# Kernel tuning notes

Measured on AMD Instinct MI355X. Metric: run time of the kernel, lower is better.

## Reference

```python
import jax, jax.numpy as jnp
import numpy as np

N, E, DIN, HID, H, ED = 50000, 800000, 128, 64, 4, 5
Z_IDX = 3          # impedance column
PHYS_W = 1.0       # physics_weight
NEG_SLOPE = 0.2    # GATv2 leaky_relu slope


def gat_layer(x, src, dst, ea, Wl, bl, Wr, br, We, att, temp, bias, concat):
    """PhysicsGATv2Conv (add_self_loops=False, eval mode / no dropout)."""
    n = x.shape[0]
    Hh, C = att.shape
    xl = (x @ Wl + bl).reshape(n, Hh, C)   # lin_l -> source features
    xr = (x @ Wr + br).reshape(n, Hh, C)   # lin_r -> target features
    # physics-enhanced edge attr: overwrite last column with temp * w / |Z|
    z = jnp.clip(ea[:, Z_IDX], 1e-6, None)
    ea = ea.at[:, -1].set(temp * PHYS_W / z)
    e = (ea @ We).reshape(-1, Hh, C)       # lin_edge (no bias)
    m = jax.nn.leaky_relu(xl[src] + xr[dst] + e, NEG_SLOPE)  # [E,H,C]
    logit = jnp.einsum('ehc,hc->eh', m, att)                 # [E,H]
    # segment softmax over incoming edges of each target node
    lmax = jax.ops.segment_max(logit, dst, num_segments=n)
    w = jnp.exp(logit - lmax[dst])
    den = jax.ops.segment_sum(w, dst, num_segments=n)
    a = w / (den[dst] + 1e-16)
    out = jax.ops.segment_sum(xl[src] * a[:, :, None], dst, num_segments=n)
    out = out.reshape(n, Hh * C) if concat else out.mean(axis=1)
    return out + bias


def layer_norm(x, w, b):
    mu = x.mean(-1, keepdims=True)
    v = ((x - mu) ** 2).mean(-1, keepdims=True)
    return (x - mu) * jax.lax.rsqrt(v + 1e-5) * w + b


def setup_inputs() -> dict:
    key = jax.random.key(0)
    ks = iter(jax.random.split(key, 40))
    nk = lambda: next(ks)
    d = {}
    d['x'] = jax.random.normal(nk(), (N, DIN), jnp.float32)
    d['edge_index'] = jax.random.randint(nk(), (2, E), 0, N)
    d['edge_attr'] = jax.random.uniform(nk(), (E, ED), jnp.float32)
    hd = HID * H
    cfg = [(DIN, True), (hd, True), (hd, False)]
    for i, (din, concat) in enumerate(cfg):
        dout = hd if concat else HID
        d[f'Wl{i}'] = jax.random.normal(nk(), (din, hd), jnp.float32) / np.sqrt(din)
        d[f'bl{i}'] = 0.01 * jax.random.normal(nk(), (hd,), jnp.float32)
        d[f'Wr{i}'] = jax.random.normal(nk(), (din, hd), jnp.float32) / np.sqrt(din)
        d[f'br{i}'] = 0.01 * jax.random.normal(nk(), (hd,), jnp.float32)
        d[f'We{i}'] = jax.random.normal(nk(), (ED, hd), jnp.float32) / np.sqrt(ED)
        d[f'att{i}'] = jax.random.normal(nk(), (H, HID), jnp.float32) / np.sqrt(HID)
        d[f'temp{i}'] = jnp.float32(1.0)
        d[f'bias{i}'] = 0.01 * jax.random.normal(nk(), (dout,), jnp.float32)
        d[f'lnw{i}'] = jnp.ones((dout,), jnp.float32)
        d[f'lnb{i}'] = jnp.zeros((dout,), jnp.float32)
    d['pw0'] = jax.random.normal(nk(), (DIN, hd), jnp.float32) / np.sqrt(DIN)
    d['pb0'] = jnp.zeros((hd,), jnp.float32)
    d['pw2'] = jax.random.normal(nk(), (hd, HID), jnp.float32) / np.sqrt(hd)
    d['pb2'] = jnp.zeros((HID,), jnp.float32)
    return d


def reference(x, edge_index, edge_attr,
              Wl0, bl0, Wr0, br0, We0, att0, temp0, bias0, lnw0, lnb0,
              Wl1, bl1, Wr1, br1, We1, att1, temp1, bias1, lnw1, lnb1,
              Wl2, bl2, Wr2, br2, We2, att2, temp2, bias2, lnw2, lnb2,
              pw0, pb0, pw2, pb2):
    src, dst = edge_index[0], edge_index[1]
    # layer 0: 128 -> 256 (concat), residual projected
    h = gat_layer(x, src, dst, edge_attr, Wl0, bl0, Wr0, br0, We0, att0, temp0, bias0, True)
    h = layer_norm(h, lnw0, lnb0) + (x @ pw0 + pb0)
    h = jax.nn.elu(h)
    # layer 1: 256 -> 256 (concat), identity residual
    h1 = gat_layer(h, src, dst, edge_attr, Wl1, bl1, Wr1, br1, We1, att1, temp1, bias1, True)
    h = layer_norm(h1, lnw1, lnb1) + h
    h = jax.nn.elu(h)
    # layer 2: 256 -> 64 (head-mean), residual projected, no activation
    h2 = gat_layer(h, src, dst, edge_attr, Wl2, bl2, Wr2, br2, We2, att2, temp2, bias2, False)
    out = layer_norm(h2, lnw2, lnb2) + (h @ pw2 + pb2)
    return out
```

## Files before the change

### kernel.cpp

```cpp
#include <hip/hip_runtime.h>
#include <math.h>

#define NN 50000
#define EE 800000
#define NB 196

typedef _Float16 half8 __attribute__((ext_vector_type(8)));
typedef _Float16 hv4  __attribute__((ext_vector_type(4)));
typedef _Float16 hv2  __attribute__((ext_vector_type(2)));
typedef __fp16 fp16v2 __attribute__((ext_vector_type(2)));
typedef float floatx16 __attribute__((ext_vector_type(16)));
typedef float fv4 __attribute__((ext_vector_type(4)));

__device__ __forceinline__ float fexp2(float x) { return __builtin_amdgcn_exp2f(x); }

template<int CTRL>
__device__ __forceinline__ float dppadd(float x) {
    int t = __builtin_amdgcn_update_dpp(0, __float_as_int(x), CTRL, 0xf, 0xf, false);
    return x + __int_as_float(t);
}
__device__ __forceinline__ float red16(float x) {
    x = dppadd<0x121>(x);
    x = dppadd<0x122>(x);
    x = dppadd<0x124>(x);
    x = dppadd<0x128>(x);
    return x;
}

__device__ __forceinline__ unsigned int dup16(float x) {
    unsigned short b = __builtin_bit_cast(unsigned short, (_Float16)x);
    return (unsigned int)b * 0x10001u;
}
__device__ __forceinline__ unsigned int duph(float x) {
#if __has_builtin(__builtin_amdgcn_cvt_pkrtz)
    fp16v2 p = __builtin_amdgcn_cvt_pkrtz(x, x);
    return __builtin_bit_cast(unsigned int, p);
#else
    return dup16(x);
#endif
}
__device__ __forceinline__ hv4 b4(unsigned int u) {
    hv2 p = __builtin_bit_cast(hv2, u);
    return (hv4){p[0], p[1], p[0], p[1]};
}
__device__ __forceinline__ float dot4h(hv4 a, hv4 b, float c) {
    hv2 al = {a[0], a[1]}, ah = {a[2], a[3]};
    hv2 bl = {b[0], b[1]}, bh = {b[2], b[3]};
#if __has_builtin(__builtin_amdgcn_fdot2)
    return __builtin_amdgcn_fdot2(al, bl, __builtin_amdgcn_fdot2(ah, bh, c, false), false);
#else
    return c + (float)a[0]*(float)b[0] + (float)a[1]*(float)b[1]
             + (float)a[2]*(float)b[2] + (float)a[3]*(float)b[3];
#endif
}

__global__ __launch_bounds__(256) void swizzleA(
    const float* __restrict__ A, _Float16* __restrict__ Asw, int M, int K)
{
    int wave = threadIdx.x >> 6, lane = threadIdx.x & 63;
    int tile = blockIdx.x;
    int kc = blockIdx.y * 4 + wave;
    int KC = K >> 4;
    if (kc >= KC) return;
    int row = tile * 32 + (lane & 31);
    int k0 = kc * 16 + (lane >> 5) * 8;
    float4 v0 = make_float4(0.f, 0.f, 0.f, 0.f);
    float4 v1 = make_float4(0.f, 0.f, 0.f, 0.f);
    if (row < M) {
        const float* p = A + (size_t)row * K + k0;
        v0 = *(const float4*)p;
        v1 = *(const float4*)(p + 4);
    }
    half8 o;
    o[0] = (_Float16)v0.x; o[1] = (_Float16)v0.y;
    o[2] = (_Float16)v0.z; o[3] = (_Float16)v0.w;
    o[4] = (_Float16)v1.x; o[5] = (_Float16)v1.y;
    o[6] = (_Float16)v1.z; o[7] = (_Float16)v1.w;
    *(half8*)(Asw + (((size_t)tile * KC + kc) * 64 + lane) * 8) = o;
}

__global__ __launch_bounds__(256) void prep_weights(
    const float* __restrict__ s0, const float* __restrict__ s1,
    const float* __restrict__ s2, const float* __restrict__ s3,
    const float* __restrict__ s4, const float* __restrict__ s5,
    const float* __restrict__ s6, const float* __restrict__ s7,
    _Float16* __restrict__ catB0, _Float16* __restrict__ catB1,
    _Float16* __restrict__ catB2,
    const float* __restrict__ bl0, const float* __restrict__ br0,
    const float* __restrict__ pb0, const float* __restrict__ bl1,
    const float* __restrict__ br1, const float* __restrict__ bl2,
    const float* __restrict__ br2, const float* __restrict__ pb2,
    float* __restrict__ cb0, float* __restrict__ cb1, float* __restrict__ cb2,
    const float* __restrict__ We0a, const float* __restrict__ We1a,
    const float* __restrict__ We2a, const float* __restrict__ att0a,
    const float* __restrict__ att1a, const float* __restrict__ att2a,
    _Float16* __restrict__ Weh)
{
    int b = blockIdx.x;
    if (b == 192) {
        const float* Ws[3] = {We0a, We1a, We2a};
        const float* As[3] = {att0a, att1a, att2a};
        for (int t = threadIdx.x; t < 4608; t += 256) {
            int l = t / 1536, o = t - l * 1536;
            float v = (o < 1280) ? Ws[l][o] : As[l][o - 1280];
            Weh[t] = (_Float16)v;
        }
        return;
    }
    if (b >= 184) {
        int t = (b - 184) * 256 + threadIdx.x;
        if (t < 768) {
            cb0[t] = (t < 256) ? bl0[t] : (t < 512) ? br0[t - 256] : pb0[t - 512];
        } else if (t < 1280) {
            int u = t - 768;
            cb1[u] = (u < 256) ? bl1[u] : br1[u - 256];
        } else if (t < 1856) {
            int u = t - 1280;
            cb2[u] = (u < 256) ? bl2[u] : (u < 512) ? br2[u - 256] : pb2[u - 512];
        }
        return;
    }
    int wave = threadIdx.x >> 6, lane = threadIdx.x & 63;
    int pair = b * 4 + wave;
    const int cum[9] = {0, 64, 128, 192, 320, 448, 576, 704, 736};
    int job = 0;
    while (pair >= cum[job + 1]) ++job;
    const float* srcs[8] = {s0, s1, s2, s3, s4, s5, s6, s7};
    const int KCs[8] = {8, 8, 8, 16, 16, 16, 16, 16};
    const int NCs[8] = {256, 256, 256, 256, 256, 256, 256, 64};
    const int ntb[8] = {0, 8, 16, 0, 8, 0, 8, 16};
    _Float16* dsts[8] = {catB0, catB0, catB0, catB1, catB1, catB2, catB2, catB2};
    int p = pair - cum[job];
    int KC = KCs[job], NC = NCs[job];
    int nt = p / KC, kc = p - nt * KC;
    int n = (nt >> 1) * 64 + ((lane & 31) * 2) + (nt & 1);
    int k0 = kc * 16 + (lane >> 5) * 8;
    const float* B = srcs[job];
    half8 o;
#pragma unroll
    for (int jj = 0; jj < 8; ++jj)
        o[jj] = (_Float16)B[(size_t)(k0 + jj) * NC + n];
    int ntG = ntb[job] + nt;
    *(half8*)(dsts[job] + (((size_t)ntG * KC + kc) * 64 + lane) * 8) = o;
}

__global__ __launch_bounds__(256) void gemm_mfma(
    const _Float16* __restrict__ Asw, const _Float16* __restrict__ Bsw,
    const float* __restrict__ bias, _Float16* __restrict__ C,
    int M, int K, int NC)
{
    const int wave = threadIdx.x >> 6, lane = threadIdx.x & 63;
    const int KC = K >> 4;
    const int rt0 = blockIdx.x * 2;
    const int NG = NC >> 6;
    int g = blockIdx.y * 4 + wave;
    if (g >= NG) g = NG - 1;

    const half8* Ap0 = (const half8*)Asw + (size_t)rt0 * KC * 64 + lane;
    const half8* Ap1 = Ap0 + (size_t)KC * 64;
    const half8* Bp0 = (const half8*)Bsw + (size_t)(2 * g) * KC * 64 + lane;
    const half8* Bp1 = Bp0 + (size_t)KC * 64;

    floatx16 accE0 = {0.f}, accE1 = {0.f}, accO0 = {0.f}, accO1 = {0.f};

#pragma unroll 4
    for (int kc = 0; kc < KC; ++kc) {
        half8 a0 = Ap0[(size_t)kc * 64];
        half8 a1 = Ap1[(size_t)kc * 64];
        half8 b0 = Bp0[(size_t)kc * 64];
        half8 b1 = Bp1[(size_t)kc * 64];
        accE0 = __builtin_amdgcn_mfma_f32_32x32x16_f16(a0, b0, accE0, 0, 0, 0);
        accE1 = __builtin_amdgcn_mfma_f32_32x32x16_f16(a1, b0, accE1, 0, 0, 0);
        accO0 = __builtin_amdgcn_mfma_f32_32x32x16_f16(a0, b1, accO0, 0, 0, 0);
        accO1 = __builtin_amdgcn_mfma_f32_32x32x16_f16(a1, b1, accO1, 0, 0, 0);
    }

    const int nlane = lane & 31, hs = lane >> 5;
    int colb = g * 64 + nlane * 2;
    float be = bias[colb], bo = bias[colb + 1];
#pragma unroll
    for (int r = 0; r < 16; ++r) {
        int rowin = (r & 3) + 8 * (r >> 2) + 4 * hs;
        int row0 = rt0 * 32 + rowin;
        int row1 = row0 + 32;
        if (row0 < M) {
            hv2 pe;
            pe[0] = (_Float16)(accE0[r] + be);
            pe[1] = (_Float16)(accO0[r] + bo);
            *(hv2*)(C + (size_t)row0 * NC + colb) = pe;
        }
        if (row1 < M) {
            hv2 po;
            po[0] = (_Float16)(accE1[r] + be);
            po[1] = (_Float16)(accO1[r] + bo);
            *(hv2*)(C + (size_t)row1 * NC + colb) = po;
        }
    }
}

__global__ __launch_bounds__(256) void hist_kernel(const int* __restrict__ dst,
                                                   int* __restrict__ deg)
{
    int e = blockIdx.x * 256 + threadIdx.x;
    if (e < EE) atomicAdd(&deg[dst[e]], 1);
}

__global__ __launch_bounds__(256) void scan_local(const int* __restrict__ deg,
                                                  int* __restrict__ rowoff,
                                                  int* __restrict__ part)
{
    __shared__ int sd[256];
    int tid = threadIdx.x;
    int i = blockIdx.x * 256 + tid;
    int v = (i < NN) ? deg[i] : 0;
    sd[tid] = v;
    __syncthreads();
    for (int off = 1; off < 256; off <<= 1) {
        int t = (tid >= off) ? sd[tid - off] : 0;
        __syncthreads();
        sd[tid] += t;
        __syncthreads();
    }
    if (i < NN) rowoff[i] = sd[tid] - v;
    if (tid == 255) part[blockIdx.x] = sd[255];
}

__global__ __launch_bounds__(256) void scan_part(int* __restrict__ part,
                                                 int* __restrict__ rowoff)
{
    __shared__ int sd[256];
    int tid = threadIdx.x;
    int v = (tid < NB) ? part[tid] : 0;
    sd[tid] = v;
    __syncthreads();
    for (int off = 1; off < 256; off <<= 1) {
        int t = (tid >= off) ? sd[tid - off] : 0;
        __syncthreads();
        sd[tid] += t;
        __syncthreads();
    }
    if (tid < NB) part[tid] = sd[tid] - v;
    if (tid == 0) rowoff[NN] = EE;
}

__global__ __launch_bounds__(256) void scan_add(int* __restrict__ rowoff,
                                                const int* __restrict__ part,
                                                int* __restrict__ cursor)
{
    int i = blockIdx.x * 256 + threadIdx.x;
    if (i < NN) {
        rowoff[i] += part[blockIdx.x];
        cursor[i] = 0;
    }
}

__global__ __launch_bounds__(256) void scatter_kernel(
    const int* __restrict__ src, const int* __restrict__ dst,
    const float* __restrict__ ea, const int* __restrict__ rowoff,
    int* __restrict__ cursor, int* __restrict__ srcp,
    unsigned int* __restrict__ apk, float* __restrict__ erec)
{
    int e = blockIdx.x * 256 + threadIdx.x;
    if (e < EE) {
        int d = dst[e];
        int pos = rowoff[d] + atomicAdd(&cursor[d], 1);
        srcp[pos] = src[e];
        const float* p = ea + (size_t)e * 5;
        uint4 o;
        o.x = dup16(p[0]); o.y = dup16(p[1]);
        o.z = dup16(p[2]); o.w = dup16(p[3]);
        *(uint4*)(apk + (size_t)pos * 4) = o;
        erec[pos] = 1.0f / fmaxf(p[3], 1e-6f);
    }
}

__global__ __launch_bounds__(256) void build_qtab(
    const float* __restrict__ erec, const float* __restrict__ temp,
    unsigned int* __restrict__ qtab)
{
    int e = blockIdx.x * 256 + threadIdx.x;
    if (e >= EE) return;
    float q = temp[0] * erec[e];
    float qs = fminf(q, 64.f);
    float inv = (q > 64.f) ? 64.f * __builtin_amdgcn_rcpf(q) : 1.0f;
    float sl = fmaxf(q * 0.015625f, 1.f) * 1.44269504088896340736f;
    uint4 o;
    o.x = dup16(qs);
    o.y = dup16(inv);
    o.z = __builtin_bit_cast(unsigned int, sl);
    o.w = 0u;
    *(uint4*)(qtab + (size_t)e * 4) = o;
}

template<int MODE, int RSTRIDE>
__global__ __launch_bounds__(256) void fused_attn_ln(
    const int* __restrict__ rowoff, const int* __restrict__ srcp,
    const unsigned int* __restrict__ apk, const unsigned int* __restrict__ qtab,
    const _Float16* __restrict__ xlp, const _Float16* __restrict__ Wh,
    const float* __restrict__ bias, const float* __restrict__ lnw,
    const float* __restrict__ lnb,
    const _Float16* __restrict__ residH, const float* __restrict__ residF,
    float* __restrict__ outF, _Float16* __restrict__ aswOut)
{
    int v = __builtin_amdgcn_readfirstlane(blockIdx.x * 4 + (threadIdx.x >> 6));
    int lane = threadIdx.x & 63;
    if (v >= NN) return;
    int grp = lane >> 4;
    int sub = lane & 15;
    int j = grp * 64 + sub * 4;

    hv4 ww0h = *(const hv4*)(Wh + j);
    hv4 ww1h = *(const hv4*)(Wh + 256 + j);
    hv4 ww2h = *(const hv4*)(Wh + 512 + j);
    hv4 ww3h = *(const hv4*)(Wh + 768 + j);
    hv4 ww4h = *(const hv4*)(Wh + 1024 + j);
    hv4 atvh = *(const hv4*)(Wh + 1280 + j);
    hv4 xrvh = *(const hv4*)(xlp + (size_t)v * RSTRIDE + 256 + j);
    const _Float16 s02 = (_Float16)0.2f;
    const hv4 sl02 = {s02, s02, s02, s02};
    const float L2E = 1.44269504088896340736f;

    float mxd = -INFINITY, dend = 0.f;
    fv4 acc = {0.f, 0.f, 0.f, 0.f};

    int beg = __builtin_amdgcn_readfirstlane(rowoff[v]);
    int end = __builtin_amdgcn_readfirstlane(rowoff[v + 1]);
    int i = beg;
    for (; i + 4 <= end; i += 4) {
        int s[4]; uint4 ap[4], qt[4]; hv4 xh[4]; float l[4];
#pragma unroll
        for (int u = 0; u < 4; ++u) {
            s[u] = __builtin_amdgcn_readfirstlane(srcp[i + u]);
            ap[u] = *(const uint4*)(apk + (size_t)(i + u) * 4);
            qt[u] = *(const uint4*)(qtab + (size_t)(i + u) * 4);
        }
#pragma unroll
        for (int u = 0; u < 4; ++u)
            xh[u] = *(const hv4*)(xlp + (size_t)s[u] * RSTRIDE + j);
#pragma unroll
        for (int u = 0; u < 4; ++u) {
            hv4 t = xh[u] + xrvh;
            t += b4(ap[u].x) * ww0h;
            t += b4(ap[u].y) * ww1h;
            t += b4(ap[u].z) * ww2h;
            t += b4(ap[u].w) * ww3h;
            hv4 m = b4(qt[u].x) * ww4h;
            m += b4(qt[u].y) * t;
            hv4 mn = m * sl02;
            m = __builtin_elementwise_max(m, mn);
            l[u] = dot4h(m, atvh, 0.f);
        }
#pragma unroll
        for (int u = 0; u < 4; ++u)
            l[u] = red16(l[u]) * __builtin_bit_cast(float, qt[u].z);
        float nm = fmaxf(fmaxf(l[0], l[1]), fmaxf(l[2], l[3]));
        nm = fmaxf(nm, mxd);
        float sc = fexp2(mxd - nm);
        float e0 = fexp2(l[0] - nm);
        float e1 = fexp2(l[1] - nm);
        float e2 = fexp2(l[2] - nm);
        float e3 = fexp2(l[3] - nm);
        mxd = nm;
        dend = dend * sc + ((e0 + e1) + (e2 + e3));
        hv4 X = xh[0] * b4(duph(e0));
        X += xh[1] * b4(duph(e1));
        X += xh[2] * b4(duph(e2));
        X += xh[3] * b4(duph(e3));
        fv4 Xf = __builtin_convertvector(X, fv4);
        acc = acc * sc + Xf;
    }
    for (; i < end; ++i) {
        int s0 = __builtin_amdgcn_readfirstlane(srcp[i]);
        uint4 ap = *(const uint4*)(apk + (size_t)i * 4);
        uint4 qt = *(const uint4*)(qtab + (size_t)i * 4);
        hv4 xh = *(const hv4*)(xlp + (size_t)s0 * RSTRIDE + j);
        hv4 t = xh + xrvh;
        t += b4(ap.x) * ww0h;
        t += b4(ap.y) * ww1h;
        t += b4(ap.z) * ww2h;
        t += b4(ap.w) * ww3h;
        hv4 m = b4(qt.x) * ww4h;
        m += b4(qt.y) * t;
        hv4 mn = m * sl02;
        m = __builtin_elementwise_max(m, mn);
        float l0 = dot4h(m, atvh, 0.f);
        l0 = red16(l0) * __builtin_bit_cast(float, qt.z);
        float nm = fmaxf(mxd, l0);
        float sc = fexp2(mxd - nm);
        float e0 = fexp2(l0 - nm);
        mxd = nm;
        dend = dend * sc + e0;
        fv4 xf = __builtin_convertvector(xh, fv4);
        acc = acc * sc + xf * e0;
    }

    float inv = __builtin_amdgcn_rcpf(dend + 1e-16f);
    if (MODE <= 1) {
        fv4 bb = *(const fv4*)(bias + j);
        fv4 o = acc * inv + bb;
        float s  = (o[0] + o[1]) + (o[2] + o[3]);
        fv4 oq = o * o;
        float s2 = (oq[0] + oq[1]) + (oq[2] + oq[3]);
        s = red16(s);   s += __shfl_xor(s, 16, 64);  s += __shfl_xor(s, 32, 64);
        s2 = red16(s2); s2 += __shfl_xor(s2, 16, 64); s2 += __shfl_xor(s2, 32, 64);
        float mu = s * (1.f / 256.f);
        float var = s2 * (1.f / 256.f) - mu * mu;
        float rs = __builtin_amdgcn_rsqf(var + 1e-5f);
        fv4 lw = *(const fv4*)(lnw + j);
        fv4 lb = *(const fv4*)(lnb + j);
        fv4 rr;
        if (MODE == 0)
            rr = __builtin_convertvector(
                *(const hv4*)(residH + (size_t)v * RSTRIDE + j), fv4);
        else
            rr = *(const fv4*)(residF + (size_t)v * 256 + j);
        fv4 y = (o - mu) * rs * lw + lb + rr;
        y[0] = (y[0] > 0.f) ? y[0] : fexp2(y[0] * L2E) - 1.f;
        y[1] = (y[1] > 0.f) ? y[1] : fexp2(y[1] * L2E) - 1.f;
        y[2] = (y[2] > 0.f) ? y[2] : fexp2(y[2] * L2E) - 1.f;
        y[3] = (y[3] > 0.f) ? y[3] : fexp2(y[3] * L2E) - 1.f;
        if (MODE == 0)
            *(fv4*)(outF + (size_t)v * 256 + j) = y;
        int kc = j >> 4, half = (j >> 3) & 1, off = j & 7;
        size_t idx = (((size_t)(v >> 5) * 16 + kc) * 64 + (v & 31) + 32 * half) * 8 + off;
        hv4 yh = __builtin_convertvector(y, hv4);
        *(hv4*)(aswOut + idx) = yh;
    } else {
        fv4 r = acc * inv;
        r[0] += __shfl_xor(r[0], 16, 64); r[0] += __shfl_xor(r[0], 32, 64);
        r[1] += __shfl_xor(r[1], 16, 64); r[1] += __shfl_xor(r[1], 32, 64);
        r[2] += __shfl_xor(r[2], 16, 64); r[2] += __shfl_xor(r[2], 32, 64);
        r[3] += __shfl_xor(r[3], 16, 64); r[3] += __shfl_xor(r[3], 32, 64);
        fv4 bb = *(const fv4*)(bias + sub * 4);
        fv4 o = r * 0.25f + bb;
        float s  = (o[0] + o[1]) + (o[2] + o[3]);
        fv4 oq = o * o;
        float s2 = (oq[0] + oq[1]) + (oq[2] + oq[3]);
        s = red16(s);
        s2 = red16(s2);
        float mu = s * (1.f / 64.f);
        float var = s2 * (1.f / 64.f) - mu * mu;
        float rs = __builtin_amdgcn_rsqf(var + 1e-5f);
        fv4 lw = *(const fv4*)(lnw + sub * 4);
        fv4 lb = *(const fv4*)(lnb + sub * 4);
        fv4 rr = __builtin_convertvector(
            *(const hv4*)(residH + (size_t)v * RSTRIDE + sub * 4), fv4);
        fv4 y = (o - mu) * rs * lw + lb + rr;
        if (grp == 0)
            *(fv4*)(outF + (size_t)v * 64 + sub * 4) = y;
    }
}

extern "C" void kernel_launch(void* const* d_in, const int* in_sizes, int n_in,
                              void* d_out, int out_size, void* d_ws, size_t ws_size,
                              hipStream_t stream)
{
    const float* x    = (const float*)d_in[0];
    const int*   eidx = (const int*)d_in[1];
    const float* ea   = (const float*)d_in[2];
    const int* src = eidx;
    const int* dst = eidx + EE;

    const float *Wl[3], *bl[3], *Wr[3], *br[3], *We[3], *att[3], *temp[3],
                *bias[3], *lnw[3], *lnb[3];
    for (int i = 0; i < 3; ++i) {
        int b = 3 + i * 10;
        Wl[i]   = (const float*)d_in[b + 0];
        bl[i]   = (const float*)d_in[b + 1];
        Wr[i]   = (const float*)d_in[b + 2];
        br[i]   = (const float*)d_in[b + 3];
        We[i]   = (const float*)d_in[b + 4];
        att[i]  = (const float*)d_in[b + 5];
        temp[i] = (const float*)d_in[b + 6];
        bias[i] = (const float*)d_in[b + 7];
        lnw[i]  = (const float*)d_in[b + 8];
        lnb[i]  = (const float*)d_in[b + 9];
    }
    const float* pw0 = (const float*)d_in[33];
    const float* pb0 = (const float*)d_in[34];
    const float* pw2 = (const float*)d_in[35];
    const float* pb2 = (const float*)d_in[36];

    char* w = (char*)d_ws;
    float* h     = (float*)w; w += (size_t)NN * 256 * 4;
    char*  gbase = w;         w += (size_t)NN * 256 * 4;
    _Float16* xlr = (_Float16*)w; w += (size_t)NN * 768 * 2;
    unsigned int* apk = (unsigned int*)w; w += (size_t)EE * 16;
    float* erec  = (float*)w; w += (size_t)EE * 4;
    int* srcp    = (int*)w;   w += (size_t)EE * 4;
    int* rowoff  = (int*)w;   w += (size_t)(NN + 16) * 4;
    int* cursor  = (int*)w;   w += (size_t)NN * 4;
    int* part    = (int*)w;   w += 1024;
    w = (char*)(((uintptr_t)w + 255) & ~(uintptr_t)255);
    _Float16* catB0 = (_Float16*)w; w += 196608;
    _Float16* catB1 = (_Float16*)w; w += 262144;
    _Float16* catB2 = (_Float16*)w; w += 294912;
    float* cb0 = (float*)w; w += 768 * 4;
    float* cb1 = (float*)w; w += 512 * 4;
    float* cb2 = (float*)w; w += 576 * 4;
    _Float16* Weh = (_Float16*)w; w += 4608 * 2;
    _Float16* Asw = (_Float16*)gbase;
    unsigned int* qtab = (unsigned int*)(gbase + 38400000);

    dim3 blk(256);
    dim3 grid_e((EE + 255) / 256);
    dim3 grid_nw((NN + 3) / 4);
    dim3 grid_nb(NB);
    const int MT2 = 782;

    hipMemsetAsync(cursor, 0, (size_t)NN * 4, stream);
    hipLaunchKernelGGL(hist_kernel, grid_e, blk, 0, stream, dst, cursor);
    hipLaunchKernelGGL(scan_local, grid_nb, blk, 0, stream, cursor, rowoff, part);
    hipLaunchKernelGGL(scan_part, dim3(1), blk, 0, stream, part, rowoff);
    hipLaunchKernelGGL(scan_add, grid_nb, blk, 0, stream, rowoff, part, cursor);
    hipLaunchKernelGGL(scatter_kernel, grid_e, blk, 0, stream,
                       src, dst, ea, rowoff, cursor, srcp, apk, erec);

    hipLaunchKernelGGL(prep_weights, dim3(193), blk, 0, stream,
                       Wl[0], Wr[0], pw0, Wl[1], Wr[1], Wl[2], Wr[2], pw2,
                       catB0, catB1, catB2,
                       bl[0], br[0], pb0, bl[1], br[1], bl[2], br[2], pb2,
                       cb0, cb1, cb2,
                       We[0], We[1], We[2], att[0], att[1], att[2], Weh);

    swizzleA<<<dim3(1564, 2), blk, 0, stream>>>(x, Asw, NN, 128);
    hipLaunchKernelGGL(build_qtab, grid_e, blk, 0, stream, erec, temp[0], qtab);
    gemm_mfma<<<dim3(MT2, 3), blk, 0, stream>>>(
        Asw, catB0, cb0, xlr, NN, 128, 768);
    fused_attn_ln<0, 768><<<grid_nw, blk, 0, stream>>>(
        rowoff, srcp, apk, qtab, xlr, Weh,
        bias[0], lnw[0], lnb[0], xlr + 512, nullptr, h, Asw);

    hipLaunchKernelGGL(build_qtab, grid_e, blk, 0, stream, erec, temp[1], qtab);
    gemm_mfma<<<dim3(MT2, 2), blk, 0, stream>>>(
        Asw, catB1, cb1, xlr, NN, 256, 512);
    fused_attn_ln<1, 512><<<grid_nw, blk, 0, stream>>>(
        rowoff, srcp, apk, qtab, xlr, Weh + 1536,
        bias[1], lnw[1], lnb[1], nullptr, h, h, Asw);

    hipLaunchKernelGGL(build_qtab, grid_e, blk, 0, stream, erec, temp[2], qtab);
    gemm_mfma<<<dim3(MT2, 3), blk, 0, stream>>>(
        Asw, catB2, cb2, xlr, NN, 256, 576);
    fused_attn_ln<2, 576><<<grid_nw, blk, 0, stream>>>(
        rowoff, srcp, apk, qtab, xlr, Weh + 3072,
        bias[2], lnw[2], lnb[2], xlr + 512, nullptr, (float*)d_out, nullptr);
}
```

Baseline: 649.0 us.

## Fold per-layer qtab build into attention kernel, pack src+erec, store residual in fp16

Removes the three build_qtab launches and their 16-byte-per-edge table, and instead computes the clamped scale, inverse and logit slope inline from temp and a reciprocal impedance. That reciprocal is packed with the source index into one int2 per edge. The layer-0 residual h is now stored in fp16 instead of fp32, halving that write and the later read. The cost is a few extra ALU ops per edge and reduced precision on the residual path.

```diff
diff --git a/kernel.cpp b/kernel.cpp
--- a/kernel.cpp
+++ b/kernel.cpp
@@ -257,49 +257,34 @@
 __global__ __launch_bounds__(256) void scatter_kernel(
     const int* __restrict__ src, const int* __restrict__ dst,
     const float* __restrict__ ea, const int* __restrict__ rowoff,
-    int* __restrict__ cursor, int* __restrict__ srcp,
-    unsigned int* __restrict__ apk, float* __restrict__ erec)
+    int* __restrict__ cursor, int2* __restrict__ sep,
+    unsigned int* __restrict__ apk)
 {
     int e = blockIdx.x * 256 + threadIdx.x;
     if (e < EE) {
         int d = dst[e];
         int pos = rowoff[d] + atomicAdd(&cursor[d], 1);
-        srcp[pos] = src[e];
         const float* p = ea + (size_t)e * 5;
+        int2 o2;
+        o2.x = src[e];
+        o2.y = __float_as_int(1.0f / fmaxf(p[3], 1e-6f));
+        sep[pos] = o2;
         uint4 o;
         o.x = dup16(p[0]); o.y = dup16(p[1]);
         o.z = dup16(p[2]); o.w = dup16(p[3]);
         *(uint4*)(apk + (size_t)pos * 4) = o;
-        erec[pos] = 1.0f / fmaxf(p[3], 1e-6f);
-    }
-}
-
-__global__ __launch_bounds__(256) void build_qtab(
-    const float* __restrict__ erec, const float* __restrict__ temp,
-    unsigned int* __restrict__ qtab)
-{
-    int e = blockIdx.x * 256 + threadIdx.x;
-    if (e >= EE) return;
-    float q = temp[0] * erec[e];
-    float qs = fminf(q, 64.f);
-    float inv = (q > 64.f) ? 64.f * __builtin_amdgcn_rcpf(q) : 1.0f;
-    float sl = fmaxf(q * 0.015625f, 1.f) * 1.44269504088896340736f;
-    uint4 o;
-    o.x = dup16(qs);
-    o.y = dup16(inv);
-    o.z = __builtin_bit_cast(unsigned int, sl);
-    o.w = 0u;
-    *(uint4*)(qtab + (size_t)e * 4) = o;
+    }
 }
 
 template<int MODE, int RSTRIDE>
 __global__ __launch_bounds__(256) void fused_attn_ln(
-    const int* __restrict__ rowoff, const int* __restrict__ srcp,
-    const unsigned int* __restrict__ apk, const unsigned int* __restrict__ qtab,
+    const int* __restrict__ rowoff, const int2* __restrict__ sep,
+    const unsigned int* __restrict__ apk,
     const _Float16* __restrict__ xlp, const _Float16* __restrict__ Wh,
+    const float* __restrict__ tmpP,
     const float* __restrict__ bias, const float* __restrict__ lnw,
     const float* __restrict__ lnb,
-    const _Float16* __restrict__ residH, const float* __restrict__ residF,
+    const _Float16* __restrict__ residH, _Float16* __restrict__ h16,
     float* __restrict__ outF, _Float16* __restrict__ aswOut)
 {
     int v = __builtin_amdgcn_readfirstlane(blockIdx.x * 4 + (threadIdx.x >> 6));
@@ -319,6 +304,7 @@
     const _Float16 s02 = (_Float16)0.2f;
     const hv4 sl02 = {s02, s02, s02, s02};
     const float L2E = 1.44269504088896340736f;
+    float tmp = tmpP[0];
 
     float mxd = -INFINITY, dend = 0.f;
     fv4 acc = {0.f, 0.f, 0.f, 0.f};
@@ -327,16 +313,26 @@
     int end = __builtin_amdgcn_readfirstlane(rowoff[v + 1]);
     int i = beg;
     for (; i + 4 <= end; i += 4) {
-        int s[4]; uint4 ap[4], qt[4]; hv4 xh[4]; float l[4];
+        int s[4]; float er[4]; uint4 ap[4]; hv4 xh[4]; float l[4];
 #pragma unroll
         for (int u = 0; u < 4; ++u) {
-            s[u] = __builtin_amdgcn_readfirstlane(srcp[i + u]);
+            int2 sv = sep[i + u];
+            s[u] = __builtin_amdgcn_readfirstlane(sv.x);
+            er[u] = __int_as_float(__builtin_amdgcn_readfirstlane(sv.y));
             ap[u] = *(const uint4*)(apk + (size_t)(i + u) * 4);
-            qt[u] = *(const uint4*)(qtab + (size_t)(i + u) * 4);
         }
 #pragma unroll
         for (int u = 0; u < 4; ++u)
             xh[u] = *(const hv4*)(xlp + (size_t)s[u] * RSTRIDE + j);
+        unsigned qpk[4], ipk[4]; float sl[4];
+#pragma unroll
+        for (int u = 0; u < 4; ++u) {
+            float q = tmp * er[u];
+            float c = fmaxf(q, 64.f);
+            qpk[u] = duph(fminf(q, 64.f));
+            ipk[u] = duph(64.f * __builtin_amdgcn_rcpf(c));
+            sl[u] = c * (L2E / 64.f);
+        }
 #pragma unroll
         for (int u = 0; u < 4; ++u) {
             hv4 t = xh[u] + xrvh;
@@ -344,15 +340,15 @@
             t += b4(ap[u].y) * ww1h;
             t += b4(ap[u].z) * ww2h;
             t += b4(ap[u].w) * ww3h;
-            hv4 m = b4(qt[u].x) * ww4h;
-            m += b4(qt[u].y) * t;
+            hv4 m = b4(qpk[u]) * ww4h;
+            m += b4(ipk[u]) * t;
             hv4 mn = m * sl02;
             m = __builtin_elementwise_max(m, mn);
             l[u] = dot4h(m, atvh, 0.f);
         }
 #pragma unroll
         for (int u = 0; u < 4; ++u)
-            l[u] = red16(l[u]) * __builtin_bit_cast(float, qt[u].z);
+            l[u] = red16(l[u]) * sl[u];
         float nm = fmaxf(fmaxf(l[0], l[1]), fmaxf(l[2], l[3]));
         nm = fmaxf(nm, mxd);
         float sc = fexp2(mxd - nm);
@@ -370,21 +366,27 @@
         acc = acc * sc + Xf;
     }
     for (; i < end; ++i) {
-        int s0 = __builtin_amdgcn_readfirstlane(srcp[i]);
+        int2 sv = sep[i];
+        int s0 = __builtin_amdgcn_readfirstlane(sv.x);
+        float er = __int_as_float(__builtin_amdgcn_readfirstlane(sv.y));
         uint4 ap = *(const uint4*)(apk + (size_t)i * 4);
-        uint4 qt = *(const uint4*)(qtab + (size_t)i * 4);
         hv4 xh = *(const hv4*)(xlp + (size_t)s0 * RSTRIDE + j);
+        float q = tmp * er;
+        float c = fmaxf(q, 64.f);
+        unsigned qpk = duph(fminf(q, 64.f));
+        unsigned ipk = duph(64.f * __builtin_amdgcn_rcpf(c));
+        float slv = c * (L2E / 64.f);
         hv4 t = xh + xrvh;
         t += b4(ap.x) * ww0h;
         t += b4(ap.y) * ww1h;
         t += b4(ap.z) * ww2h;
         t += b4(ap.w) * ww3h;
-        hv4 m = b4(qt.x) * ww4h;
-        m += b4(qt.y) * t;
+        hv4 m = b4(qpk) * ww4h;
+        m += b4(ipk) * t;
         hv4 mn = m * sl02;
         m = __builtin_elementwise_max(m, mn);
         float l0 = dot4h(m, atvh, 0.f);
-        l0 = red16(l0) * __builtin_bit_cast(float, qt.z);
+        l0 = red16(l0) * slv;
         float nm = fmaxf(mxd, l0);
         float sc = fexp2(mxd - nm);
         float e0 = fexp2(l0 - nm);
@@ -413,17 +415,18 @@
             rr = __builtin_convertvector(
                 *(const hv4*)(residH + (size_t)v * RSTRIDE + j), fv4);
         else
-            rr = *(const fv4*)(residF + (size_t)v * 256 + j);
+            rr = __builtin_convertvector(
+                *(const hv4*)(residH + (size_t)v * 256 + j), fv4);
         fv4 y = (o - mu) * rs * lw + lb + rr;
         y[0] = (y[0] > 0.f) ? y[0] : fexp2(y[0] * L2E) - 1.f;
         y[1] = (y[1] > 0.f) ? y[1] : fexp2(y[1] * L2E) - 1.f;
         y[2] = (y[2] > 0.f) ? y[2] : fexp2(y[2] * L2E) - 1.f;
         y[3] = (y[3] > 0.f) ? y[3] : fexp2(y[3] * L2E) - 1.f;
+        hv4 yh = __builtin_convertvector(y, hv4);
         if (MODE == 0)
-            *(fv4*)(outF + (size_t)v * 256 + j) = y;
+            *(hv4*)(h16 + (size_t)v * 256 + j) = yh;
         int kc = j >> 4, half = (j >> 3) & 1, off = j & 7;
         size_t idx = (((size_t)(v >> 5) * 16 + kc) * 64 + (v & 31) + 32 * half) * 8 + off;
-        hv4 yh = __builtin_convertvector(y, hv4);
         *(hv4*)(aswOut + idx) = yh;
     } else {
         fv4 r = acc * inv;
@@ -482,12 +485,11 @@
     const float* pb2 = (const float*)d_in[36];
 
     char* w = (char*)d_ws;
-    float* h     = (float*)w; w += (size_t)NN * 256 * 4;
+    _Float16* h16 = (_Float16*)w; w += (size_t)NN * 256 * 2;
     char*  gbase = w;         w += (size_t)NN * 256 * 4;
     _Float16* xlr = (_Float16*)w; w += (size_t)NN * 768 * 2;
     unsigned int* apk = (unsigned int*)w; w += (size_t)EE * 16;
-    float* erec  = (float*)w; w += (size_t)EE * 4;
-    int* srcp    = (int*)w;   w += (size_t)EE * 4;
+    int2* sep    = (int2*)w;  w += (size_t)EE * 8;
     int* rowoff  = (int*)w;   w += (size_t)(NN + 16) * 4;
     int* cursor  = (int*)w;   w += (size_t)NN * 4;
     int* part    = (int*)w;   w += 1024;
@@ -500,7 +502,6 @@
     float* cb2 = (float*)w; w += 576 * 4;
     _Float16* Weh = (_Float16*)w; w += 4608 * 2;
     _Float16* Asw = (_Float16*)gbase;
-    unsigned int* qtab = (unsigned int*)(gbase + 38400000);
 
     dim3 blk(256);
     dim3 grid_e((EE + 255) / 256);
@@ -514,7 +515,7 @@
     hipLaunchKernelGGL(scan_part, dim3(1), blk, 0, stream, part, rowoff);
     hipLaunchKernelGGL(scan_add, grid_nb, blk, 0, stream, rowoff, part, cursor);
     hipLaunchKernelGGL(scatter_kernel, grid_e, blk, 0, stream,
-                       src, dst, ea, rowoff, cursor, srcp, apk, erec);
+                       src, dst, ea, rowoff, cursor, sep, apk);
 
     hipLaunchKernelGGL(prep_weights, dim3(193), blk, 0, stream,
                        Wl[0], Wr[0], pw0, Wl[1], Wr[1], Wl[2], Wr[2], pw2,
@@ -524,24 +525,21 @@
                        We[0], We[1], We[2], att[0], att[1], att[2], Weh);
 
     swizzleA<<<dim3(1564, 2), blk, 0, stream>>>(x, Asw, NN, 128);
-    hipLaunchKernelGGL(build_qtab, grid_e, blk, 0, stream, erec, temp[0], qtab);
     gemm_mfma<<<dim3(MT2, 3), blk, 0, stream>>>(
         Asw, catB0, cb0, xlr, NN, 128, 768);
     fused_attn_ln<0, 768><<<grid_nw, blk, 0, stream>>>(
-        rowoff, srcp, apk, qtab, xlr, Weh,
-        bias[0], lnw[0], lnb[0], xlr + 512, nullptr, h, Asw);
-
-    hipLaunchKernelGGL(build_qtab, grid_e, blk, 0, stream, erec, temp[1], qtab);
+        rowoff, sep, apk, xlr, Weh, temp[0],
+        bias[0], lnw[0], lnb[0], xlr + 512, h16, nullptr, Asw);
+
     gemm_mfma<<<dim3(MT2, 2), blk, 0, stream>>>(
         Asw, catB1, cb1, xlr, NN, 256, 512);
     fused_attn_ln<1, 512><<<grid_nw, blk, 0, stream>>>(
-        rowoff, srcp, apk, qtab, xlr, Weh + 1536,
-        bias[1], lnw[1], lnb[1], nullptr, h, h, Asw);
-
-    hipLaunchKernelGGL(build_qtab, grid_e, blk, 0, stream, erec, temp[2], qtab);
+        rowoff, sep, apk, xlr, Weh + 1536, temp[1],
+        bias[1], lnw[1], lnb[1], h16, nullptr, nullptr, Asw);
+
     gemm_mfma<<<dim3(MT2, 3), blk, 0, stream>>>(
         Asw, catB2, cb2, xlr, NN, 256, 576);
     fused_attn_ln<2, 576><<<grid_nw, blk, 0, stream>>>(
-        rowoff, srcp, apk, qtab, xlr, Weh + 3072,
+        rowoff, sep, apk, xlr, Weh + 3072, temp[2],
         bias[2], lnw[2], lnb[2], xlr + 512, nullptr, (float*)d_out, nullptr);
 }
```

Result: faster. 626.4 us (-3.5%).

## Pack src with reciprocal impedance, merge qtab builds, store residual as fp16

Applied to the files above, without the earlier changes.

Packs the source index and the reciprocal impedance into one int2 per edge, replacing the separate srcp and erec arrays. Two of the three build_qtab launches are merged into one kernel that writes two tables, and the table for layer 2 is built into the same slot after layer 0 has consumed it. The layer-1 residual h is now kept in fp16 instead of fp32, which halves its write and read traffic. The costs are an extra 4 bytes read per edge in the attention loop (the unused .y field), slightly lower residual precision, and a dependency on workspace offsets not overlapping.

```diff
diff --git a/kernel.cpp b/kernel.cpp
--- a/kernel.cpp
+++ b/kernel.cpp
@@ -257,49 +257,67 @@
 __global__ __launch_bounds__(256) void scatter_kernel(
     const int* __restrict__ src, const int* __restrict__ dst,
     const float* __restrict__ ea, const int* __restrict__ rowoff,
-    int* __restrict__ cursor, int* __restrict__ srcp,
-    unsigned int* __restrict__ apk, float* __restrict__ erec)
+    int* __restrict__ cursor, int2* __restrict__ sep,
+    unsigned int* __restrict__ apk)
 {
     int e = blockIdx.x * 256 + threadIdx.x;
     if (e < EE) {
         int d = dst[e];
         int pos = rowoff[d] + atomicAdd(&cursor[d], 1);
-        srcp[pos] = src[e];
         const float* p = ea + (size_t)e * 5;
+        int2 o2;
+        o2.x = src[e];
+        o2.y = __float_as_int(1.0f / fmaxf(p[3], 1e-6f));
+        sep[pos] = o2;
         uint4 o;
         o.x = dup16(p[0]); o.y = dup16(p[1]);
         o.z = dup16(p[2]); o.w = dup16(p[3]);
         *(uint4*)(apk + (size_t)pos * 4) = o;
-        erec[pos] = 1.0f / fmaxf(p[3], 1e-6f);
     }
 }
 
 __global__ __launch_bounds__(256) void build_qtab(
-    const float* __restrict__ erec, const float* __restrict__ temp,
-    unsigned int* __restrict__ qtab)
+    const int2* __restrict__ sep,
+    const float* __restrict__ tA, unsigned int* __restrict__ qA,
+    const float* __restrict__ tB, unsigned int* __restrict__ qB)
 {
     int e = blockIdx.x * 256 + threadIdx.x;
     if (e >= EE) return;
-    float q = temp[0] * erec[e];
-    float qs = fminf(q, 64.f);
-    float inv = (q > 64.f) ? 64.f * __builtin_amdgcn_rcpf(q) : 1.0f;
-    float sl = fmaxf(q * 0.015625f, 1.f) * 1.44269504088896340736f;
-    uint4 o;
-    o.x = dup16(qs);
-    o.y = dup16(inv);
-    o.z = __builtin_bit_cast(unsigned int, sl);
-    o.w = 0u;
-    *(uint4*)(qtab + (size_t)e * 4) = o;
+    float er = __int_as_float(sep[e].y);
+    {
+        float q = tA[0] * er;
+        float qs = fminf(q, 64.f);
+        float inv = (q > 64.f) ? 64.f * __builtin_amdgcn_rcpf(q) : 1.0f;
+        float sl = fmaxf(q * 0.015625f, 1.f) * 1.44269504088896340736f;
+        uint4 o;
+        o.x = dup16(qs);
+        o.y = dup16(inv);
+        o.z = __builtin_bit_cast(unsigned int, sl);
+        o.w = 0u;
+        *(uint4*)(qA + (size_t)e * 4) = o;
+    }
+    if (qB) {
+        float q = tB[0] * er;
+        float qs = fminf(q, 64.f);
+        float inv = (q > 64.f) ? 64.f * __builtin_amdgcn_rcpf(q) : 1.0f;
+        float sl = fmaxf(q * 0.015625f, 1.f) * 1.44269504088896340736f;
+        uint4 o;
+        o.x = dup16(qs);
+        o.y = dup16(inv);
+        o.z = __builtin_bit_cast(unsigned int, sl);
+        o.w = 0u;
+        *(uint4*)(qB + (size_t)e * 4) = o;
+    }
 }
 
 template<int MODE, int RSTRIDE>
 __global__ __launch_bounds__(256) void fused_attn_ln(
-    const int* __restrict__ rowoff, const int* __restrict__ srcp,
+    const int* __restrict__ rowoff, const int2* __restrict__ sep,
     const unsigned int* __restrict__ apk, const unsigned int* __restrict__ qtab,
     const _Float16* __restrict__ xlp, const _Float16* __restrict__ Wh,
     const float* __restrict__ bias, const float* __restrict__ lnw,
     const float* __restrict__ lnb,
-    const _Float16* __restrict__ residH, const float* __restrict__ residF,
+    const _Float16* __restrict__ residH, _Float16* __restrict__ h16,
     float* __restrict__ outF, _Float16* __restrict__ aswOut)
 {
     int v = __builtin_amdgcn_readfirstlane(blockIdx.x * 4 + (threadIdx.x >> 6));
@@ -330,7 +348,8 @@
         int s[4]; uint4 ap[4], qt[4]; hv4 xh[4]; float l[4];
 #pragma unroll
         for (int u = 0; u < 4; ++u) {
-            s[u] = __builtin_amdgcn_readfirstlane(srcp[i + u]);
+            int2 sv = sep[i + u];
+            s[u] = __builtin_amdgcn_readfirstlane(sv.x);
             ap[u] = *(const uint4*)(apk + (size_t)(i + u) * 4);
             qt[u] = *(const uint4*)(qtab + (size_t)(i + u) * 4);
         }
@@ -370,7 +389,8 @@
         acc = acc * sc + Xf;
     }
     for (; i < end; ++i) {
-        int s0 = __builtin_amdgcn_readfirstlane(srcp[i]);
+        int2 sv = sep[i];
+        int s0 = __builtin_amdgcn_readfirstlane(sv.x);
         uint4 ap = *(const uint4*)(apk + (size_t)i * 4);
         uint4 qt = *(const uint4*)(qtab + (size_t)i * 4);
         hv4 xh = *(const hv4*)(xlp + (size_t)s0 * RSTRIDE + j);
@@ -413,17 +433,18 @@
             rr = __builtin_convertvector(
                 *(const hv4*)(residH + (size_t)v * RSTRIDE + j), fv4);
         else
-            rr = *(const fv4*)(residF + (size_t)v * 256 + j);
+            rr = __builtin_convertvector(
+                *(const hv4*)(residH + (size_t)v * 256 + j), fv4);
         fv4 y = (o - mu) * rs * lw + lb + rr;
         y[0] = (y[0] > 0.f) ? y[0] : fexp2(y[0] * L2E) - 1.f;
         y[1] = (y[1] > 0.f) ? y[1] : fexp2(y[1] * L2E) - 1.f;
         y[2] = (y[2] > 0.f) ? y[2] : fexp2(y[2] * L2E) - 1.f;
         y[3] = (y[3] > 0.f) ? y[3] : fexp2(y[3] * L2E) - 1.f;
+        hv4 yh = __builtin_convertvector(y, hv4);
         if (MODE == 0)
-            *(fv4*)(outF + (size_t)v * 256 + j) = y;
+            *(hv4*)(h16 + (size_t)v * 256 + j) = yh;
         int kc = j >> 4, half = (j >> 3) & 1, off = j & 7;
         size_t idx = (((size_t)(v >> 5) * 16 + kc) * 64 + (v & 31) + 32 * half) * 8 + off;
-        hv4 yh = __builtin_convertvector(y, hv4);
         *(hv4*)(aswOut + idx) = yh;
     } else {
         fv4 r = acc * inv;
@@ -482,12 +503,12 @@
     const float* pb2 = (const float*)d_in[36];
 
     char* w = (char*)d_ws;
-    float* h     = (float*)w; w += (size_t)NN * 256 * 4;
+    _Float16* h16 = (_Float16*)w; w += (size_t)NN * 256 * 2;
     char*  gbase = w;         w += (size_t)NN * 256 * 4;
     _Float16* xlr = (_Float16*)w; w += (size_t)NN * 768 * 2;
     unsigned int* apk = (unsigned int*)w; w += (size_t)EE * 16;
-    float* erec  = (float*)w; w += (size_t)EE * 4;
-    int* srcp    = (int*)w;   w += (size_t)EE * 4;
+    int2* sep    = (int2*)w;  w += (size_t)EE * 8;
+    unsigned int* qtab1 = (unsigned int*)w; w += (size_t)EE * 16;
     int* rowoff  = (int*)w;   w += (size_t)(NN + 16) * 4;
     int* cursor  = (int*)w;   w += (size_t)NN * 4;
     int* part    = (int*)w;   w += 1024;
@@ -500,7 +521,7 @@
     float* cb2 = (float*)w; w += 576 * 4;
     _Float16* Weh = (_Float16*)w; w += 4608 * 2;
     _Float16* Asw = (_Float16*)gbase;
-    unsigned int* qtab = (unsigned int*)(gbase + 38400000);
+    unsigned int* qslot = (unsigned int*)(gbase + 26000000);
 
     dim3 blk(256);
     dim3 grid_e((EE + 255) / 256);
@@ -514,7 +535,10 @@
     hipLaunchKernelGGL(scan_part, dim3(1), blk, 0, stream, part, rowoff);
     hipLaunchKernelGGL(scan_add, grid_nb, blk, 0, stream, rowoff, part, cursor);
     hipLaunchKernelGGL(scatter_kernel, grid_e, blk, 0, stream,
-                       src, dst, ea, rowoff, cursor, srcp, apk, erec);
+                       src, dst, ea, rowoff, cursor, sep, apk);
+
+    hipLaunchKernelGGL(build_qtab, grid_e, blk, 0, stream,
+                       sep, temp[0], qslot, temp[1], qtab1);
 
     hipLaunchKernelGGL(prep_weights, dim3(193), blk, 0, stream,
                        Wl[0], Wr[0], pw0, Wl[1], Wr[1], Wl[2], Wr[2], pw2,
@@ -524,24 +548,24 @@
                        We[0], We[1], We[2], att[0], att[1], att[2], Weh);
 
     swizzleA<<<dim3(1564, 2), blk, 0, stream>>>(x, Asw, NN, 128);
-    hipLaunchKernelGGL(build_qtab, grid_e, blk, 0, stream, erec, temp[0], qtab);
     gemm_mfma<<<dim3(MT2, 3), blk, 0, stream>>>(
         Asw, catB0, cb0, xlr, NN, 128, 768);
     fused_attn_ln<0, 768><<<grid_nw, blk, 0, stream>>>(
-        rowoff, srcp, apk, qtab, xlr, Weh,
-        bias[0], lnw[0], lnb[0], xlr + 512, nullptr, h, Asw);
-
-    hipLaunchKernelGGL(build_qtab, grid_e, blk, 0, stream, erec, temp[1], qtab);
+        rowoff, sep, apk, qslot, xlr, Weh,
+        bias[0], lnw[0], lnb[0], xlr + 512, h16, nullptr, Asw);
+
+    hipLaunchKernelGGL(build_qtab, grid_e, blk, 0, stream,
+                       sep, temp[2], qslot, nullptr, nullptr);
+
     gemm_mfma<<<dim3(MT2, 2), blk, 0, stream>>>(
         Asw, catB1, cb1, xlr, NN, 256, 512);
     fused_attn_ln<1, 512><<<grid_nw, blk, 0, stream>>>(
-        rowoff, srcp, apk, qtab, xlr, Weh + 1536,
-        bias[1], lnw[1], lnb[1], nullptr, h, h, Asw);
-
-    hipLaunchKernelGGL(build_qtab, grid_e, blk, 0, stream, erec, temp[2], qtab);
+        rowoff, sep, apk, qtab1, xlr, Weh + 1536,
+        bias[1], lnw[1], lnb[1], h16, nullptr, nullptr, Asw);
+
     gemm_mfma<<<dim3(MT2, 3), blk, 0, stream>>>(
         Asw, catB2, cb2, xlr, NN, 256, 576);
     fused_attn_ln<2, 576><<<grid_nw, blk, 0, stream>>>(
-        rowoff, srcp, apk, qtab, xlr, Weh + 3072,
+        rowoff, sep, apk, qslot, xlr, Weh + 3072,
         bias[2], lnw[2], lnb[2], xlr + 512, nullptr, (float*)d_out, nullptr);
 }
```

After: 615.6 us, median of 2. 5.1% less time.
